# Performance work log

Measured on AMD Instinct MI355X. Metric: run time of the kernel, lower is better.

Reference implementation:

```python
import jax, jax.numpy as jnp
import numpy as np
import math

D_MODEL = 2048
NUM_HEADS = 16
D_FF = 8192
HEAD_DIM = D_MODEL // NUM_HEADS
EPS = 1e-5


def _xavier(key, out_f, in_f):
    std = math.sqrt(2.0 / (in_f + out_f))
    return jax.random.normal(key, (out_f, in_f), dtype=jnp.float32) * std


def setup_inputs() -> dict:
    key = jax.random.key(0)
    ks = jax.random.split(key, 8)
    x = jax.random.normal(ks[0], (2, 2048, D_MODEL), dtype=jnp.float32)
    return {
        "x": x,
        "Wq": _xavier(ks[1], D_MODEL, D_MODEL),
        "Wk": _xavier(ks[2], D_MODEL, D_MODEL),
        "Wv": _xavier(ks[3], D_MODEL, D_MODEL),
        "Wo": _xavier(ks[4], D_MODEL, D_MODEL),
        "W1": _xavier(ks[5], D_FF, D_MODEL),
        "W2": _xavier(ks[6], D_MODEL, D_FF),
        "g1": jnp.ones((D_MODEL,), jnp.float32),
        "b1": jnp.zeros((D_MODEL,), jnp.float32),
        "g2": jnp.ones((D_MODEL,), jnp.float32),
        "b2": jnp.zeros((D_MODEL,), jnp.float32),
    }


def _ternary(w):
    # per-tensor abs-mean threshold -> {-1, 0, 1}
    abs_w = jnp.abs(w)
    thr = jnp.mean(abs_w)
    return jnp.where(abs_w > thr, jnp.sign(w), jnp.zeros_like(w))


def _tlin(x, w):
    # F.linear with ternarized weight [out, in], no bias
    return jnp.einsum("bsi,oi->bso", x, _ternary(w))


def _layernorm(x, g, b):
    mu = jnp.mean(x, axis=-1, keepdims=True)
    var = jnp.mean(jnp.square(x - mu), axis=-1, keepdims=True)
    return (x - mu) * jax.lax.rsqrt(var + EPS) * g + b


def reference(x, Wq, Wk, Wv, Wo, W1, W2, g1, b1, g2, b2):
    B, S, D = x.shape
    H, Hd = NUM_HEADS, HEAD_DIM
    q = _tlin(x, Wq).reshape(B, S, H, Hd).transpose(0, 2, 1, 3)  # bhsd
    k = _tlin(x, Wk).reshape(B, S, H, Hd).transpose(0, 2, 1, 3)
    v = _tlin(x, Wv).reshape(B, S, H, Hd).transpose(0, 2, 1, 3)
    scores = jnp.einsum("bhqd,bhkd->bhqk", q, k) / math.sqrt(Hd)
    probs = jax.nn.softmax(scores, axis=-1)
    attn = jnp.einsum("bhqk,bhkd->bhqd", probs, v)
    attn = attn.transpose(0, 2, 1, 3).reshape(B, S, D)
    attn = _tlin(attn, Wo)
    x = _layernorm(x + attn, g1, b1)  # dropout is identity in eval
    ff = _tlin(jax.nn.relu(_tlin(x, W1)), W2)
    x = _layernorm(x + ff, g2, b2)
    return x
```

## Files before the change

### kernel.cpp

```cpp
#include <hip/hip_runtime.h>
#include <hip/hip_bf16.h>

typedef __bf16 bf16_t;
typedef __bf16 bf16x8 __attribute__((ext_vector_type(8)));
typedef __bf16 bf16x4 __attribute__((ext_vector_type(4)));
typedef float f32x4 __attribute__((ext_vector_type(4)));
typedef int i32x4 __attribute__((ext_vector_type(4)));

__device__ __forceinline__ f32x4 mfma16(bf16x8 a, bf16x8 b, f32x4 c) {
  return __builtin_amdgcn_mfma_f32_16x16x32_bf16(a, b, c, 0, 0, 0);
}

__device__ __forceinline__ void gload16(const void* g, void* l) {
  __builtin_amdgcn_global_load_lds(
      (const __attribute__((address_space(1))) void*)g,
      (__attribute__((address_space(3))) void*)l, 16, 0, 0);
}

__global__ void abssum_all(const float* __restrict__ W0, const float* __restrict__ W1_,
                           const float* __restrict__ W2_, const float* __restrict__ W3,
                           const float* __restrict__ W4, const float* __restrict__ W5,
                           double* __restrict__ partial) {
  __shared__ double sd[256];
  const int w = blockIdx.y, tid = threadIdx.x;
  const float* W = (w == 0) ? W0 : (w == 1) ? W1_ : (w == 2) ? W2_ : (w == 3) ? W3 : (w == 4) ? W4 : W5;
  const int n4 = (w < 4) ? 1048576 : 4194304;
  double s = 0.0;
  for (int i = blockIdx.x * 256 + tid; i < n4; i += 262144) {
    float4 v = ((const float4*)W)[i];
    s += (double)fabsf(v.x); s += (double)fabsf(v.y);
    s += (double)fabsf(v.z); s += (double)fabsf(v.w);
  }
  sd[tid] = s; __syncthreads();
  for (int st = 128; st > 0; st >>= 1) { if (tid < st) sd[tid] += sd[tid + st]; __syncthreads(); }
  if (tid == 0) partial[w * 1024 + blockIdx.x] = sd[0];
}

__global__ void abssum_fin(const double* __restrict__ partial, double* __restrict__ sums) {
  __shared__ double sd[256];
  const int tid = threadIdx.x;
  const double* p = partial + blockIdx.x * 1024;
  double s = p[tid] + p[tid + 256] + p[tid + 512] + p[tid + 768];
  sd[tid] = s; __syncthreads();
  for (int st = 128; st > 0; st >>= 1) { if (tid < st) sd[tid] += sd[tid + st]; __syncthreads(); }
  if (tid == 0) sums[blockIdx.x] = sd[0];
}

__global__ void ternarize_k(const float* __restrict__ W, bf16_t* __restrict__ out,
                            const double* __restrict__ sum, double n) {
  const double thr = sum[0] / n;
  const int i = blockIdx.x * 256 + threadIdx.x;
  float4 v = ((const float4*)W)[i];
  bf16x4 o;
  float t;
  t = ((double)fabsf(v.x) > thr) ? (v.x > 0.f ? 1.f : -1.f) : 0.f; o[0] = (bf16_t)t;
  t = ((double)fabsf(v.y) > thr) ? (v.y > 0.f ? 1.f : -1.f) : 0.f; o[1] = (bf16_t)t;
  t = ((double)fabsf(v.z) > thr) ? (v.z > 0.f ? 1.f : -1.f) : 0.f; o[2] = (bf16_t)t;
  t = ((double)fabsf(v.w) > thr) ? (v.w > 0.f ? 1.f : -1.f) : 0.f; o[3] = (bf16_t)t;
  *(bf16x4*)&out[(size_t)i * 4] = o;
}

__global__ void split_x_k(const float* __restrict__ X, bf16_t* __restrict__ xh, bf16_t* __restrict__ xl) {
  const int i = blockIdx.x * 256 + threadIdx.x;
  float4 v = ((const float4*)X)[i];
  bf16x4 h, l;
  h[0] = (bf16_t)v.x; l[0] = (bf16_t)(v.x - (float)h[0]);
  h[1] = (bf16_t)v.y; l[1] = (bf16_t)(v.y - (float)h[1]);
  h[2] = (bf16_t)v.z; l[2] = (bf16_t)(v.z - (float)h[2]);
  h[3] = (bf16_t)v.w; l[3] = (bf16_t)(v.w - (float)h[3]);
  *(bf16x4*)&xh[(size_t)i * 4] = h;
  *(bf16x4*)&xl[(size_t)i * 4] = l;
}

template <int EPI, bool SPLITA>
__global__ __launch_bounds__(512, 2) void gemmP(
    const bf16_t* __restrict__ Ah, const bf16_t* __restrict__ Al,
    const bf16_t* __restrict__ Bw,
    void* __restrict__ C0, void* __restrict__ C1,
    int M, int N, int K) {
  constexpr int BM = SPLITA ? 64 : 128;
  constexpr int MREP = SPLITA ? 2 : 4;
  constexpr int ABUF = BM * 64;
  constexpr int BBUF = 256 * 64;
  __shared__ __align__(16) bf16_t sA[3][ABUF];
  __shared__ __align__(16) bf16_t sA2[SPLITA ? 3 : 1][SPLITA ? ABUF : 8];
  __shared__ __align__(16) bf16_t sB[3][BBUF];

  const int tid = threadIdx.x;
  const int wid = tid >> 6, lane = tid & 63, lr = lane & 15, lg = lane >> 4;
  const int wr = wid >> 2, wc = wid & 3;
  const size_t Ks = (size_t)K;

  const int nwg = gridDim.x * gridDim.y;
  const int bid0 = blockIdx.y * gridDim.x + blockIdx.x;
  const int swz = (bid0 & 7) * (nwg >> 3) + (bid0 >> 3);
  const int bx = swz % gridDim.x, by = swz / gridDim.x;
  const size_t m0 = (size_t)by * BM, n0 = (size_t)bx * 256;
  const int nt = K / 64;

  f32x4 acc[MREP][4] = {};

  auto STAGEH = [&](int bi, int kt, int half) {
    const size_t ko = (size_t)kt * 64;
    if (half == 0) {
#pragma unroll
      for (int i = 0; i < BM / 64; i++) {
        const int t = i * 512 + tid;
        const int r = t >> 3;
        const int su = (t & 7) ^ (r & 7);
        const int lo = (i * 512 + wid * 64) * 8;
        gload16(Ah + (m0 + r) * Ks + ko + su * 8, (void*)&sA[bi][lo]);
        if constexpr (SPLITA) gload16(Al + (m0 + r) * Ks + ko + su * 8, (void*)&sA2[bi][lo]);
      }
      {
        const int r = tid >> 3;
        const int su = (tid & 7) ^ (r & 7);
        gload16(Bw + (n0 + r) * Ks + ko + su * 8, (void*)&sB[bi][(wid * 64) * 8]);
      }
    } else {
#pragma unroll
      for (int i = 1; i < 4; i++) {
        const int t = i * 512 + tid;
        const int r = t >> 3;
        const int su = (t & 7) ^ (r & 7);
        gload16(Bw + (n0 + r) * Ks + ko + su * 8, (void*)&sB[bi][(i * 512 + wid * 64) * 8]);
      }
    }
  };
  auto LDA = [&](const bf16_t* base, int m, int k) -> bf16x8 {
    const int row = wr * (BM / 2) + m * 16 + lr;
    const int u = (k * 4 + lg) ^ (lr & 7);
    return *(const bf16x8*)&base[row * 64 + u * 8];
  };
  auto LDB = [&](const bf16_t* base, int n, int k) -> bf16x8 {
    const int row = wc * 64 + n * 16 + lr;
    const int u = (k * 4 + lg) ^ (lr & 7);
    return *(const bf16x8*)&base[row * 64 + u * 8];
  };

  STAGEH(0, 0, 0); STAGEH(0, 0, 1);
  STAGEH(1, 1, 0); STAGEH(1, 1, 1);
  asm volatile("s_waitcnt vmcnt(6)" ::: "memory");
  __builtin_amdgcn_s_barrier();

  int bc = 0, bs = 2;
  for (int kt = 0; kt < nt; kt++) {
    const bool pf = (kt + 2 < nt);
    bf16x8 a[MREP][2], bfr[4][2];
#pragma unroll
    for (int m = 0; m < MREP; m++)
#pragma unroll
      for (int k = 0; k < 2; k++) a[m][k] = LDA(&sA[bc][0], m, k);
    if constexpr (SPLITA) {
#pragma unroll
      for (int n = 0; n < 4; n++)
#pragma unroll
        for (int k = 0; k < 2; k++) bfr[n][k] = LDB(&sB[bc][0], n, k);
    } else {
#pragma unroll
      for (int n = 0; n < 2; n++)
#pragma unroll
        for (int k = 0; k < 2; k++) bfr[n][k] = LDB(&sB[bc][0], n, k);
    }
    if (pf) STAGEH(bs, kt + 2, 0);
    __builtin_amdgcn_s_barrier();
    asm volatile("s_waitcnt lgkmcnt(0)" ::: "memory");
    __builtin_amdgcn_sched_barrier(0);
    __builtin_amdgcn_s_setprio(1);
    if constexpr (SPLITA) {
#pragma unroll
      for (int k = 0; k < 2; k++)
#pragma unroll
        for (int m = 0; m < MREP; m++)
#pragma unroll
          for (int n = 0; n < 4; n++) acc[m][n] = mfma16(a[m][k], bfr[n][k], acc[m][n]);
    } else {
#pragma unroll
      for (int k = 0; k < 2; k++)
#pragma unroll
        for (int m = 0; m < MREP; m++)
#pragma unroll
          for (int n = 0; n < 2; n++) acc[m][n] = mfma16(a[m][k], bfr[n][k], acc[m][n]);
    }
    __builtin_amdgcn_s_setprio(0);
    __builtin_amdgcn_s_barrier();
    if constexpr (SPLITA) {
#pragma unroll
      for (int m = 0; m < MREP; m++)
#pragma unroll
        for (int k = 0; k < 2; k++) a[m][k] = LDA(&sA2[bc][0], m, k);
    } else {
#pragma unroll
      for (int n = 0; n < 2; n++)
#pragma unroll
        for (int k = 0; k < 2; k++) bfr[n + 2][k] = LDB(&sB[bc][0], n + 2, k);
    }
    if (pf) STAGEH(bs, kt + 2, 1);
    if (kt + 1 < nt) {
      if (pf) asm volatile("s_waitcnt vmcnt(6)" ::: "memory");
      else    asm volatile("s_waitcnt vmcnt(0)" ::: "memory");
    }
    __builtin_amdgcn_s_barrier();
    asm volatile("s_waitcnt lgkmcnt(0)" ::: "memory");
    __builtin_amdgcn_sched_barrier(0);
    __builtin_amdgcn_s_setprio(1);
    if constexpr (SPLITA) {
#pragma unroll
      for (int k = 0; k < 2; k++)
#pragma unroll
        for (int m = 0; m < MREP; m++)
#pragma unroll
          for (int n = 0; n < 4; n++) acc[m][n] = mfma16(a[m][k], bfr[n][k], acc[m][n]);
    } else {
#pragma unroll
      for (int k = 0; k < 2; k++)
#pragma unroll
        for (int m = 0; m < MREP; m++)
#pragma unroll
          for (int n = 0; n < 2; n++) acc[m][n + 2] = mfma16(a[m][k], bfr[n + 2][k], acc[m][n + 2]);
    }
    __builtin_amdgcn_s_setprio(0);
    __builtin_amdgcn_s_barrier();
    bc = (bc + 1 == 3) ? 0 : bc + 1;
    bs = (bs + 1 == 3) ? 0 : bs + 1;
  }

  const int row0 = (int)m0 + wr * (BM / 2), colb = (int)n0 + wc * 64;
#pragma unroll
  for (int m = 0; m < MREP; m++)
#pragma unroll
    for (int n = 0; n < 4; n++)
#pragma unroll
      for (int j = 0; j < 4; j++) {
        const int r = row0 + m * 16 + lg * 4 + j;
        const int c = colb + n * 16 + lr;
        const float v = acc[m][n][j];
        if constexpr (EPI == 0) {
          bf16_t hi = (bf16_t)v;
          ((bf16_t*)C0)[(size_t)r * N + c] = hi;
          ((bf16_t*)C1)[(size_t)r * N + c] = (bf16_t)(v - (float)hi);
        } else if constexpr (EPI == 1) {
          const int bb = r >> 11, ss = r & 2047;
          ((bf16_t*)C0)[((size_t)bb * 2048 + c) * 2048 + ss] = (bf16_t)v;
        } else if constexpr (EPI == 2) {
          ((float*)C0)[(size_t)r * N + c] = v;
        } else {
          ((bf16_t*)C0)[(size_t)r * N + c] = (bf16_t)fmaxf(v, 0.f);
        }
      }
  (void)M;
}

__global__ __launch_bounds__(256, 2) void attn_k(
    const bf16_t* __restrict__ qh, const bf16_t* __restrict__ ql,
    const bf16_t* __restrict__ kh, const bf16_t* __restrict__ kl,
    const bf16_t* __restrict__ vT, bf16_t* __restrict__ out) {
  __shared__ __align__(16) bf16_t sKh[2 * 8192];
  __shared__ __align__(16) bf16_t sKl[2 * 8192];
  __shared__ __align__(16) bf16_t plds[4][2048];

  const int fid = blockIdx.y * 16 + blockIdx.x;
  const int qt = fid >> 5;
  const int bh = (fid & 7) * 4 + ((fid >> 3) & 3);
  const int b = bh >> 4, h = bh & 15;
  const int wv = threadIdx.x >> 6, lane = threadIdx.x & 63, lr = lane & 15, lg = lane >> 4;
  const size_t tok0 = (size_t)b * 2048 + qt * 128 + wv * 16;
  bf16_t* pw = &plds[wv][0];

  auto STAGE = [&](int bufi, int kv0n) {
#pragma unroll
    for (int i = 0; i < 4; i++) {
      const int tt = wv * 4 + i;
      const int r = tt * 4 + (lane >> 4);
      const int ce = ((lane & 15) ^ (r & 7)) * 8;
      const size_t gofs = ((size_t)b * 2048 + kv0n + r) * 2048 + h * 128 + ce;
      gload16(kh + gofs, (void*)&sKh[bufi * 8192 + tt * 512]);
      gload16(kl + gofs, (void*)&sKl[bufi * 8192 + tt * 512]);
    }
  };

  bf16x8 qhf[2][4], qlf[2][4];
#pragma unroll
  for (int t = 0; t < 2; t++) {
    const bf16_t* qp = qh + (tok0 + t * 64 + lr) * 2048 + h * 128 + lg * 8;
    const bf16_t* qp2 = ql + (tok0 + t * 64 + lr) * 2048 + h * 128 + lg * 8;
#pragma unroll
    for (int ks = 0; ks < 4; ks++) {
      qhf[t][ks] = *(const bf16x8*)(qp + ks * 32);
      qlf[t][ks] = *(const bf16x8*)(qp2 + ks * 32);
    }
  }
  f32x4 oacc[2][8] = {};
  float mrun[2] = {-1e30f, -1e30f};
  float lrun[2] = {0.f, 0.f};
  const bf16_t* vbase = vT + ((size_t)b * 2048 + h * 128) * 2048;
  const float sc = 0.08838834764831845f;
  const int swz8 = 2 * (lr & 7);

  STAGE(0, 0);
  for (int c = 0; c < 32; c++) {
    const int kv0 = c * 64;
    if (c + 1 < 32) {
      STAGE((c + 1) & 1, kv0 + 64);
      asm volatile("s_waitcnt vmcnt(8)" ::: "memory");
    } else {
      asm volatile("s_waitcnt vmcnt(0)" ::: "memory");
    }
    __builtin_amdgcn_s_barrier();

    const int bufo = (c & 1) * 8192;
    f32x4 s[2][4] = {};
#pragma unroll
    for (int nb = 0; nb < 4; nb++) {
      const int rbase = bufo + (nb * 16 + lr) * 128;
#pragma unroll
      for (int ks = 0; ks < 4; ks++) {
        const int u = (((ks * 4 + lg) ^ (lr & 7)) * 8);
        bf16x8 kf = *(const bf16x8*)&sKh[rbase + u];
        bf16x8 kg = *(const bf16x8*)&sKl[rbase + u];
        s[0][nb] = mfma16(kf, qhf[0][ks], s[0][nb]);
        s[1][nb] = mfma16(kf, qhf[1][ks], s[1][nb]);
        s[0][nb] = mfma16(kf, qlf[0][ks], s[0][nb]);
        s[1][nb] = mfma16(kf, qlf[1][ks], s[1][nb]);
        s[0][nb] = mfma16(kg, qhf[0][ks], s[0][nb]);
        s[1][nb] = mfma16(kg, qhf[1][ks], s[1][nb]);
      }
    }

    float resc[2];
#pragma unroll
    for (int t = 0; t < 2; t++) {
#pragma unroll
      for (int nb = 0; nb < 4; nb++) s[t][nb] *= sc;
      f32x4 m4 = s[t][0];
      m4 = __builtin_elementwise_max(m4, s[t][1]);
      m4 = __builtin_elementwise_max(m4, s[t][2]);
      m4 = __builtin_elementwise_max(m4, s[t][3]);
      float mx = fmaxf(fmaxf(m4[0], m4[1]), fmaxf(m4[2], m4[3]));
      mx = fmaxf(mx, __shfl_xor(mx, 16));
      mx = fmaxf(mx, __shfl_xor(mx, 32));
      const float mnew = fmaxf(mrun[t], mx);
      resc[t] = __expf(mrun[t] - mnew);
      mrun[t] = mnew;
      float ls = 0.f;
#pragma unroll
      for (int nb = 0; nb < 4; nb++) {
        bf16x4 pk;
#pragma unroll
        for (int j = 0; j < 4; j++) {
          const float p = __expf(s[t][nb][j] - mnew);
          ls += p;
          pk[j] = (bf16_t)p;
        }
        const int s8 = (4 * nb + lg) ^ swz8;
        *(bf16x4*)&pw[t * 1024 + lr * 64 + s8 * 4] = pk;
      }
      ls += __shfl_xor(ls, 16);
      ls += __shfl_xor(ls, 32);
      lrun[t] = lrun[t] * resc[t] + ls;
    }
#pragma unroll
    for (int dt = 0; dt < 8; dt++) {
      oacc[0][dt] *= resc[0];
      oacc[1][dt] *= resc[1];
    }

    bf16x8 pfr[2][2];
#pragma unroll
    for (int t = 0; t < 2; t++)
#pragma unroll
      for (int kc = 0; kc < 2; kc++) {
        const int se = (8 * kc + 2 * lg) ^ swz8;
        pfr[t][kc] = *(const bf16x8*)&pw[t * 1024 + lr * 64 + se * 4];
      }

    const bf16_t* vp = vbase + kv0 + lg * 8;
#pragma unroll
    for (int dt = 0; dt < 8; dt++) {
      const bf16_t* vr = vp + (size_t)(dt * 16 + lr) * 2048;
      bf16x8 v0 = *(const bf16x8*)(vr);
      bf16x8 v1 = *(const bf16x8*)(vr + 32);
      oacc[0][dt] = mfma16(v0, pfr[0][0], oacc[0][dt]);
      oacc[1][dt] = mfma16(v0, pfr[1][0], oacc[1][dt]);
      oacc[0][dt] = mfma16(v1, pfr[0][1], oacc[0][dt]);
      oacc[1][dt] = mfma16(v1, pfr[1][1], oacc[1][dt]);
    }
    asm volatile("" ::: "memory");
    __builtin_amdgcn_s_barrier();
  }

  asm volatile("s_waitcnt lgkmcnt(0)" ::: "memory");
#pragma unroll
  for (int t = 0; t < 2; t++) {
    bf16_t* ep = &sKh[wv * 4096 + t * 2048];
    const float inv = 1.f / lrun[t];
#pragma unroll
    for (int dt = 0; dt < 8; dt++) {
      bf16x4 pk;
#pragma unroll
      for (int j = 0; j < 4; j++) pk[j] = (bf16_t)(oacc[t][dt][j] * inv);
      const int s5 = (4 * dt + lg) ^ swz8;
      *(bf16x4*)&ep[lr * 128 + s5 * 4] = pk;
    }
  }
  asm volatile("s_waitcnt lgkmcnt(0)" ::: "memory");
  {
    const int q = lane >> 2, c4 = lane & 3;
    const int qs = 2 * (q & 7);
#pragma unroll
    for (int t = 0; t < 2; t++) {
      const bf16_t* ep = &sKh[wv * 4096 + t * 2048];
      bf16_t* orow = out + (tok0 + t * 64 + q) * 2048 + h * 128 + c4 * 32;
#pragma unroll
      for (int i = 0; i < 4; i++) {
        const int se = (c4 * 8 + 2 * i) ^ qs;
        bf16x8 vv = *(const bf16x8*)&ep[q * 128 + se * 4];
        *(bf16x8*)(orow + i * 8) = vv;
      }
    }
  }
}

__global__ __launch_bounds__(256) void ln_k(
    const float* __restrict__ X, const float* __restrict__ R,
    const float* __restrict__ G, const float* __restrict__ Bt,
    float* __restrict__ O32, bf16_t* __restrict__ O16) {
  const int t = blockIdx.x, tid = threadIdx.x;
  const float4* xp = (const float4*)(X + (size_t)t * 2048);
  const float4* rp = (const float4*)(R + (size_t)t * 2048);
  float4 v0 = xp[tid], w0 = rp[tid];
  float4 v1 = xp[tid + 256], w1 = rp[tid + 256];
  v0.x += w0.x; v0.y += w0.y; v0.z += w0.z; v0.w += w0.w;
  v1.x += w1.x; v1.y += w1.y; v1.z += w1.z; v1.w += w1.w;
  float sum = v0.x + v0.y + v0.z + v0.w + v1.x + v1.y + v1.z + v1.w;
  float sq = v0.x * v0.x + v0.y * v0.y + v0.z * v0.z + v0.w * v0.w +
             v1.x * v1.x + v1.y * v1.y + v1.z * v1.z + v1.w * v1.w;
  for (int d = 1; d < 64; d <<= 1) { sum += __shfl_xor(sum, d); sq += __shfl_xor(sq, d); }
  __shared__ float s1[4], s2[4];
  const int wv = tid >> 6, lane = tid & 63;
  if (lane == 0) { s1[wv] = sum; s2[wv] = sq; }
  __syncthreads();
  const float tot = s1[0] + s1[1] + s1[2] + s1[3];
  const float tsq = s2[0] + s2[1] + s2[2] + s2[3];
  const float mu = tot * (1.f / 2048.f);
  const float var = tsq * (1.f / 2048.f) - mu * mu;
  const float rs = 1.f / sqrtf(var + 1e-5f);
  const float4* gp = (const float4*)G;
  const float4* bp = (const float4*)Bt;
  float4 g0 = gp[tid], g1v = gp[tid + 256], b0 = bp[tid], b1v = bp[tid + 256];
  float4 o0, o1;
  o0.x = (v0.x - mu) * rs * g0.x + b0.x; o0.y = (v0.y - mu) * rs * g0.y + b0.y;
  o0.z = (v0.z - mu) * rs * g0.z + b0.z; o0.w = (v0.w - mu) * rs * g0.w + b0.w;
  o1.x = (v1.x - mu) * rs * g1v.x + b1v.x; o1.y = (v1.y - mu) * rs * g1v.y + b1v.y;
  o1.z = (v1.z - mu) * rs * g1v.z + b1v.z; o1.w = (v1.w - mu) * rs * g1v.w + b1v.w;
  ((float4*)(O32 + (size_t)t * 2048))[tid] = o0;
  ((float4*)(O32 + (size_t)t * 2048))[tid + 256] = o1;
  if (O16) {
    bf16x4 h0, h1;
    h0[0] = (bf16_t)o0.x; h0[1] = (bf16_t)o0.y; h0[2] = (bf16_t)o0.z; h0[3] = (bf16_t)o0.w;
    h1[0] = (bf16_t)o1.x; h1[1] = (bf16_t)o1.y; h1[2] = (bf16_t)o1.z; h1[3] = (bf16_t)o1.w;
    *(bf16x4*)&O16[(size_t)t * 2048 + tid * 4] = h0;
    *(bf16x4*)&O16[(size_t)t * 2048 + 1024 + tid * 4] = h1;
  }
}

extern "C" void kernel_launch(void* const* d_in, const int* in_sizes, int n_in,
                              void* d_out, int out_size, void* d_ws, size_t ws_size,
                              hipStream_t stream) {
  const float* x  = (const float*)d_in[0];
  const float* Wq = (const float*)d_in[1];
  const float* Wk = (const float*)d_in[2];
  const float* Wv = (const float*)d_in[3];
  const float* Wo = (const float*)d_in[4];
  const float* W1 = (const float*)d_in[5];
  const float* W2 = (const float*)d_in[6];
  const float* g1 = (const float*)d_in[7];
  const float* b1 = (const float*)d_in[8];
  const float* g2 = (const float*)d_in[9];
  const float* b2 = (const float*)d_in[10];
  float* out = (float*)d_out;
  char* ws = (char*)d_ws;

  constexpr size_t SZB = (size_t)4096 * 2048 * 2;
  bf16_t* xh = (bf16_t*)(ws + 0 * SZB);
  bf16_t* xl = (bf16_t*)(ws + 1 * SZB);
  bf16_t* qh = (bf16_t*)(ws + 2 * SZB);
  bf16_t* ql = (bf16_t*)(ws + 3 * SZB);
  bf16_t* kh = (bf16_t*)(ws + 4 * SZB);
  bf16_t* kl = (bf16_t*)(ws + 5 * SZB);
  bf16_t* vt = (bf16_t*)(ws + 6 * SZB);
  bf16_t* at = (bf16_t*)(ws + 7 * SZB);
  float* o32 = (float*)(ws + 8 * SZB);
  bf16_t* wt = (bf16_t*)(ws + 8 * SZB + (size_t)4096 * 2048 * 4);
  double* red = (double*)(ws + 8 * SZB + (size_t)4096 * 2048 * 4 + (size_t)8192 * 2048 * 2);
  double* sums = red + 8192;
  float* h1 = (float*)ws;
  bf16_t* h1b = qh;
  bf16_t* f1 = kh;
  float* g32 = o32;
  (void)in_sizes; (void)n_in; (void)out_size; (void)ws_size;

  abssum_all<<<dim3(1024, 6), 256, 0, stream>>>(Wq, Wk, Wv, Wo, W1, W2, red);
  abssum_fin<<<6, 256, 0, stream>>>(red, sums);
  split_x_k<<<8192, 256, 0, stream>>>(x, xh, xl);

  ternarize_k<<<4096, 256, 0, stream>>>(Wq, wt, sums + 0, 4194304.0);
  gemmP<0, true><<<dim3(8, 64), 512, 0, stream>>>(xh, xl, wt, qh, ql, 4096, 2048, 2048);
  ternarize_k<<<4096, 256, 0, stream>>>(Wk, wt, sums + 1, 4194304.0);
  gemmP<0, true><<<dim3(8, 64), 512, 0, stream>>>(xh, xl, wt, kh, kl, 4096, 2048, 2048);
  ternarize_k<<<4096, 256, 0, stream>>>(Wv, wt, sums + 2, 4194304.0);
  gemmP<1, false><<<dim3(8, 32), 512, 0, stream>>>(xh, nullptr, wt, vt, nullptr, 4096, 2048, 2048);
  attn_k<<<dim3(16, 32), 256, 0, stream>>>(qh, ql, kh, kl, vt, at);
  ternarize_k<<<4096, 256, 0, stream>>>(Wo, wt, sums + 3, 4194304.0);
  gemmP<2, false><<<dim3(8, 32), 512, 0, stream>>>(at, nullptr, wt, o32, nullptr, 4096, 2048, 2048);
  ln_k<<<4096, 256, 0, stream>>>(x, o32, g1, b1, h1, h1b);
  ternarize_k<<<16384, 256, 0, stream>>>(W1, wt, sums + 4, 16777216.0);
  gemmP<3, false><<<dim3(32, 32), 512, 0, stream>>>(h1b, nullptr, wt, f1, nullptr, 4096, 8192, 2048);
  ternarize_k<<<16384, 256, 0, stream>>>(W2, wt, sums + 5, 16777216.0);
  gemmP<2, false><<<dim3(8, 32), 512, 0, stream>>>(f1, nullptr, wt, g32, nullptr, 4096, 2048, 8192);
  ln_k<<<4096, 256, 0, stream>>>(h1, g32, g2, b2, out, nullptr);
}
```

Measured before the change: 881.4 us.

## Fuse Q/K projections into one GEMM and add lazy softmax rescale in attention

Ternarizes Wq and Wk into adjacent halves of the weight buffer and runs one N=4096 GEMM that writes an interleaved QK buffer, so the attention kernel reads Q and K with row stride 4096. This removes one GEMM launch and wave tail. Inside attention it also skips the running-max update and accumulator rescale when the block max grows by at most 8, and raises wave priority around the MFMA loops. It also shrinks and pads the per-wave P and epilogue LDS buffers. Lazy rescaling lets unnormalised exponentials reach up to e^8 before correction, which narrows numeric headroom in bf16/fp32.

```diff
diff --git a/kernel.cpp b/kernel.cpp
--- a/kernel.cpp
+++ b/kernel.cpp
@@ -257,7 +257,7 @@
     const bf16_t* __restrict__ vT, bf16_t* __restrict__ out) {
   __shared__ __align__(16) bf16_t sKh[2 * 8192];
   __shared__ __align__(16) bf16_t sKl[2 * 8192];
-  __shared__ __align__(16) bf16_t plds[4][2048];
+  __shared__ __align__(16) bf16_t plds[4][1168];
 
   const int fid = blockIdx.y * 16 + blockIdx.x;
   const int qt = fid >> 5;
@@ -273,7 +273,7 @@
       const int tt = wv * 4 + i;
       const int r = tt * 4 + (lane >> 4);
       const int ce = ((lane & 15) ^ (r & 7)) * 8;
-      const size_t gofs = ((size_t)b * 2048 + kv0n + r) * 2048 + h * 128 + ce;
+      const size_t gofs = ((size_t)b * 2048 + kv0n + r) * 4096 + h * 128 + ce;
       gload16(kh + gofs, (void*)&sKh[bufi * 8192 + tt * 512]);
       gload16(kl + gofs, (void*)&sKl[bufi * 8192 + tt * 512]);
     }
@@ -282,8 +282,8 @@
   bf16x8 qhf[2][4], qlf[2][4];
 #pragma unroll
   for (int t = 0; t < 2; t++) {
-    const bf16_t* qp = qh + (tok0 + t * 64 + lr) * 2048 + h * 128 + lg * 8;
-    const bf16_t* qp2 = ql + (tok0 + t * 64 + lr) * 2048 + h * 128 + lg * 8;
+    const bf16_t* qp = qh + (tok0 + t * 64 + lr) * 4096 + h * 128 + lg * 8;
+    const bf16_t* qp2 = ql + (tok0 + t * 64 + lr) * 4096 + h * 128 + lg * 8;
 #pragma unroll
     for (int ks = 0; ks < 4; ks++) {
       qhf[t][ks] = *(const bf16x8*)(qp + ks * 32);
@@ -310,6 +310,7 @@
 
     const int bufo = (c & 1) * 8192;
     f32x4 s[2][4] = {};
+    __builtin_amdgcn_s_setprio(1);
 #pragma unroll
     for (int nb = 0; nb < 4; nb++) {
       const int rbase = bufo + (nb * 16 + lr) * 128;
@@ -326,55 +327,64 @@
         s[1][nb] = mfma16(kg, qhf[1][ks], s[1][nb]);
       }
     }
-
+    __builtin_amdgcn_s_setprio(0);
+
+    bf16x8 pfr[2][2];
     float resc[2];
+    bool skip[2];
 #pragma unroll
     for (int t = 0; t < 2; t++) {
 #pragma unroll
       for (int nb = 0; nb < 4; nb++) s[t][nb] *= sc;
-      f32x4 m4 = s[t][0];
-      m4 = __builtin_elementwise_max(m4, s[t][1]);
-      m4 = __builtin_elementwise_max(m4, s[t][2]);
-      m4 = __builtin_elementwise_max(m4, s[t][3]);
+      f32x4 m4 = __builtin_elementwise_max(
+          __builtin_elementwise_max(s[t][0], s[t][1]),
+          __builtin_elementwise_max(s[t][2], s[t][3]));
       float mx = fmaxf(fmaxf(m4[0], m4[1]), fmaxf(m4[2], m4[3]));
       mx = fmaxf(mx, __shfl_xor(mx, 16));
       mx = fmaxf(mx, __shfl_xor(mx, 32));
-      const float mnew = fmaxf(mrun[t], mx);
-      resc[t] = __expf(mrun[t] - mnew);
-      mrun[t] = mnew;
+      skip[t] = (__all(mx <= mrun[t] + 8.f) != 0);
+      float rs_ = 1.f;
+      if (!skip[t]) {
+        const float mnew = fmaxf(mrun[t], mx);
+        rs_ = __expf(mrun[t] - mnew);
+        mrun[t] = mnew;
+      }
+      resc[t] = rs_;
       float ls = 0.f;
 #pragma unroll
       for (int nb = 0; nb < 4; nb++) {
         bf16x4 pk;
 #pragma unroll
         for (int j = 0; j < 4; j++) {
-          const float p = __expf(s[t][nb][j] - mnew);
+          const float p = __expf(s[t][nb][j] - mrun[t]);
           ls += p;
           pk[j] = (bf16_t)p;
         }
         const int s8 = (4 * nb + lg) ^ swz8;
-        *(bf16x4*)&pw[t * 1024 + lr * 64 + s8 * 4] = pk;
+        *(bf16x4*)&pw[lr * 72 + s8 * 4] = pk;
       }
       ls += __shfl_xor(ls, 16);
       ls += __shfl_xor(ls, 32);
-      lrun[t] = lrun[t] * resc[t] + ls;
-    }
-#pragma unroll
-    for (int dt = 0; dt < 8; dt++) {
-      oacc[0][dt] *= resc[0];
-      oacc[1][dt] *= resc[1];
-    }
-
-    bf16x8 pfr[2][2];
-#pragma unroll
-    for (int t = 0; t < 2; t++)
+      lrun[t] = lrun[t] * rs_ + ls;
+      asm volatile("s_waitcnt lgkmcnt(0)" ::: "memory");
+      __builtin_amdgcn_sched_barrier(0);
 #pragma unroll
       for (int kc = 0; kc < 2; kc++) {
         const int se = (8 * kc + 2 * lg) ^ swz8;
-        pfr[t][kc] = *(const bf16x8*)&pw[t * 1024 + lr * 64 + se * 4];
-      }
+        pfr[t][kc] = *(const bf16x8*)&pw[lr * 72 + se * 4];
+      }
+    }
+    if (!skip[0]) {
+#pragma unroll
+      for (int dt = 0; dt < 8; dt++) oacc[0][dt] *= resc[0];
+    }
+    if (!skip[1]) {
+#pragma unroll
+      for (int dt = 0; dt < 8; dt++) oacc[1][dt] *= resc[1];
+    }
 
     const bf16_t* vp = vbase + kv0 + lg * 8;
+    __builtin_amdgcn_s_setprio(1);
 #pragma unroll
     for (int dt = 0; dt < 8; dt++) {
       const bf16_t* vr = vp + (size_t)(dt * 16 + lr) * 2048;
@@ -385,38 +395,36 @@
       oacc[0][dt] = mfma16(v1, pfr[0][1], oacc[0][dt]);
       oacc[1][dt] = mfma16(v1, pfr[1][1], oacc[1][dt]);
     }
+    __builtin_amdgcn_s_setprio(0);
     asm volatile("" ::: "memory");
     __builtin_amdgcn_s_barrier();
   }
 
-  asm volatile("s_waitcnt lgkmcnt(0)" ::: "memory");
-#pragma unroll
-  for (int t = 0; t < 2; t++) {
-    bf16_t* ep = &sKh[wv * 4096 + t * 2048];
-    const float inv = 1.f / lrun[t];
-#pragma unroll
-    for (int dt = 0; dt < 8; dt++) {
-      bf16x4 pk;
-#pragma unroll
-      for (int j = 0; j < 4; j++) pk[j] = (bf16_t)(oacc[t][dt][j] * inv);
-      const int s5 = (4 * dt + lg) ^ swz8;
-      *(bf16x4*)&ep[lr * 128 + s5 * 4] = pk;
-    }
-  }
-  asm volatile("s_waitcnt lgkmcnt(0)" ::: "memory");
   {
+    bf16_t* ep = &sKh[wv * 2176];
     const int q = lane >> 2, c4 = lane & 3;
     const int qs = 2 * (q & 7);
 #pragma unroll
     for (int t = 0; t < 2; t++) {
-      const bf16_t* ep = &sKh[wv * 4096 + t * 2048];
+      const float inv = 1.f / lrun[t];
+#pragma unroll
+      for (int dt = 0; dt < 8; dt++) {
+        bf16x4 pk;
+#pragma unroll
+        for (int j = 0; j < 4; j++) pk[j] = (bf16_t)(oacc[t][dt][j] * inv);
+        const int s5 = (4 * dt + lg) ^ swz8;
+        *(bf16x4*)&ep[lr * 136 + s5 * 4] = pk;
+      }
+      asm volatile("s_waitcnt lgkmcnt(0)" ::: "memory");
+      __builtin_amdgcn_sched_barrier(0);
       bf16_t* orow = out + (tok0 + t * 64 + q) * 2048 + h * 128 + c4 * 32;
 #pragma unroll
       for (int i = 0; i < 4; i++) {
         const int se = (c4 * 8 + 2 * i) ^ qs;
-        bf16x8 vv = *(const bf16x8*)&ep[q * 128 + se * 4];
+        bf16x8 vv = *(const bf16x8*)&ep[q * 136 + se * 4];
         *(bf16x8*)(orow + i * 8) = vv;
       }
+      asm volatile("s_waitcnt lgkmcnt(0)" ::: "memory");
     }
   }
 }
@@ -482,21 +490,19 @@
   char* ws = (char*)d_ws;
 
   constexpr size_t SZB = (size_t)4096 * 2048 * 2;
-  bf16_t* xh = (bf16_t*)(ws + 0 * SZB);
-  bf16_t* xl = (bf16_t*)(ws + 1 * SZB);
-  bf16_t* qh = (bf16_t*)(ws + 2 * SZB);
-  bf16_t* ql = (bf16_t*)(ws + 3 * SZB);
-  bf16_t* kh = (bf16_t*)(ws + 4 * SZB);
-  bf16_t* kl = (bf16_t*)(ws + 5 * SZB);
-  bf16_t* vt = (bf16_t*)(ws + 6 * SZB);
-  bf16_t* at = (bf16_t*)(ws + 7 * SZB);
-  float* o32 = (float*)(ws + 8 * SZB);
-  bf16_t* wt = (bf16_t*)(ws + 8 * SZB + (size_t)4096 * 2048 * 4);
+  bf16_t* xh  = (bf16_t*)(ws + 0 * SZB);
+  bf16_t* xl  = (bf16_t*)(ws + 1 * SZB);
+  bf16_t* qkh = (bf16_t*)(ws + 2 * SZB);
+  bf16_t* qkl = (bf16_t*)(ws + 4 * SZB);
+  bf16_t* vt  = (bf16_t*)(ws + 6 * SZB);
+  bf16_t* at  = (bf16_t*)(ws + 7 * SZB);
+  float* o32  = (float*)(ws + 8 * SZB);
+  bf16_t* wt  = (bf16_t*)(ws + 8 * SZB + (size_t)4096 * 2048 * 4);
   double* red = (double*)(ws + 8 * SZB + (size_t)4096 * 2048 * 4 + (size_t)8192 * 2048 * 2);
   double* sums = red + 8192;
   float* h1 = (float*)ws;
-  bf16_t* h1b = qh;
-  bf16_t* f1 = kh;
+  bf16_t* h1b = qkh;
+  bf16_t* f1 = (bf16_t*)(ws + 4 * SZB);
   float* g32 = o32;
   (void)in_sizes; (void)n_in; (void)out_size; (void)ws_size;
 
@@ -505,12 +511,11 @@
   split_x_k<<<8192, 256, 0, stream>>>(x, xh, xl);
 
   ternarize_k<<<4096, 256, 0, stream>>>(Wq, wt, sums + 0, 4194304.0);
-  gemmP<0, true><<<dim3(8, 64), 512, 0, stream>>>(xh, xl, wt, qh, ql, 4096, 2048, 2048);
-  ternarize_k<<<4096, 256, 0, stream>>>(Wk, wt, sums + 1, 4194304.0);
-  gemmP<0, true><<<dim3(8, 64), 512, 0, stream>>>(xh, xl, wt, kh, kl, 4096, 2048, 2048);
+  ternarize_k<<<4096, 256, 0, stream>>>(Wk, wt + 4194304, sums + 1, 4194304.0);
+  gemmP<0, true><<<dim3(16, 64), 512, 0, stream>>>(xh, xl, wt, qkh, qkl, 4096, 4096, 2048);
   ternarize_k<<<4096, 256, 0, stream>>>(Wv, wt, sums + 2, 4194304.0);
   gemmP<1, false><<<dim3(8, 32), 512, 0, stream>>>(xh, nullptr, wt, vt, nullptr, 4096, 2048, 2048);
-  attn_k<<<dim3(16, 32), 256, 0, stream>>>(qh, ql, kh, kl, vt, at);
+  attn_k<<<dim3(16, 32), 256, 0, stream>>>(qkh, qkl, qkh + 2048, qkl + 2048, vt, at);
   ternarize_k<<<4096, 256, 0, stream>>>(Wo, wt, sums + 3, 4194304.0);
   gemmP<2, false><<<dim3(8, 32), 512, 0, stream>>>(at, nullptr, wt, o32, nullptr, 4096, 2048, 2048);
   ln_k<<<4096, 256, 0, stream>>>(x, o32, g1, b1, h1, h1b);
```

After: 893.1 us. Within noise of the previous version (+1.3%).
